# Performance work log

Hardware: AMD Instinct MI355X
Metric: run time of the kernel (lower is better)

Reference implementation:

```python
import jax, jax.numpy as jnp
import numpy as np

LAMBDA_VOLUME = 0.2
LAMBDA_WEIGHTED_ADJ = 0.15
LAMBDA_SYM = 0.05
AGE_MAX = 100.0
EPS_ROW = 1e-8
EPS_STD = 1e-6


def _smooth_l1(x):
    # F.smooth_l1_loss(x, 0) with beta=1, mean reduction
    ax = jnp.abs(x)
    return jnp.mean(jnp.where(ax < 1.0, 0.5 * x * x, ax - 0.5))


def setup_inputs() -> dict:
    key = jax.random.key(0)
    ks = jax.random.split(key, 9)
    B, C, X = 2, 32, 96
    logits = jax.random.normal(ks[0], (B, C, X, X, X), dtype=jnp.float32)
    age = jax.random.uniform(ks[1], (B, 1), dtype=jnp.float32) * AGE_MAX
    w_young = jax.random.uniform(ks[2], (C, C), dtype=jnp.float32)
    w_old = jax.random.uniform(ks[3], (C, C), dtype=jnp.float32)
    # expected per-class volumes ~ total_voxels / C in scale
    vol_means_young = jax.random.uniform(ks[4], (C,), dtype=jnp.float32) * 50000.0
    vol_means_old = jax.random.uniform(ks[5], (C,), dtype=jnp.float32) * 50000.0
    vol_stds_young = jax.random.uniform(ks[6], (C,), dtype=jnp.float32) * 5000.0 + 1000.0
    vol_stds_old = jax.random.uniform(ks[7], (C,), dtype=jnp.float32) * 5000.0 + 1000.0
    prior_adj = jax.random.uniform(ks[8], (C, C), dtype=jnp.float32)
    # left-right pair permutation: class i <-> i + C//2
    perm = jnp.concatenate([jnp.arange(C // 2, C), jnp.arange(0, C // 2)]).astype(jnp.int64)
    return {"logits": logits, "age": age, "w_young": w_young, "w_old": w_old,
            "vol_means_young": vol_means_young, "vol_means_old": vol_means_old,
            "vol_stds_young": vol_stds_young, "vol_stds_old": vol_stds_old,
            "prior_adj": prior_adj, "perm": perm}


def reference(logits, age, w_young, w_old, vol_means_young, vol_means_old,
              vol_stds_young, vol_stds_old, prior_adj, perm):
    B, C = logits.shape[0], logits.shape[1]
    probs = jax.nn.softmax(logits, axis=1)  # (B,C,X,Y,Z)
    alpha = jnp.clip(age / AGE_MAX, 0.0, 1.0)  # (B,1) interpolation between age anchors

    # ---- weighted adjacency loss (temperature == 1.0 -> no pow) ----
    pf = probs.reshape(B, C, -1)                     # (B,C,N)
    A = jnp.einsum('bcn,bdn->bcd', pf, pf)           # bmm(probs, probs^T)
    A = A * (1.0 - jnp.eye(C, dtype=A.dtype))        # zero diagonal
    W = (1.0 - alpha)[:, :, None] * w_young[None] + alpha[:, :, None] * w_old[None]  # (B,C,C)
    A = A * W
    Aw = A.mean(axis=0)
    Aw = Aw / jnp.clip(Aw.sum(axis=1, keepdims=True), EPS_ROW)
    prior = prior_adj * (1.0 - jnp.eye(C, dtype=prior_adj.dtype))
    prior = prior / jnp.clip(prior.sum(axis=1, keepdims=True), EPS_ROW)
    loss_adj = jnp.mean(jnp.abs(Aw - prior))

    # ---- volume consistency loss ----
    pred_vol = probs.sum(axis=(2, 3, 4))             # (B,C)
    means = (1.0 - alpha) * vol_means_young[None] + alpha * vol_means_old[None]
    stds = (1.0 - alpha) * vol_stds_young[None] + alpha * vol_stds_old[None]
    loss_vol = _smooth_l1((pred_vol - means) / (stds + EPS_STD))

    # ---- symmetry consistency loss (flip along X axis = dim 2, swap LR pairs) ----
    p_flip = jnp.flip(probs, axis=2)
    p_swap = p_flip[:, perm]                         # channel permutation = pairwise swap
    loss_sym = jnp.mean(jnp.abs(probs - p_swap))

    total = (LAMBDA_WEIGHTED_ADJ * loss_adj
             + LAMBDA_VOLUME * loss_vol
             + LAMBDA_SYM * loss_sym)
    return total
```

## Files before the change

kernel.cpp:

```cpp
#include <hip/hip_runtime.h>
#include <math.h>

#define CX 32
#define XX 9216
#define X3 884736
#define TILE_PAIRS 128
#define TILES_PER_B 3456
#define BLOCKS_PER_B 384
#define STRIDE 257


__global__ __launch_bounds__(256, 3)
void main_pass(const float* __restrict__ logits,
               float* __restrict__ A_acc,
               float* __restrict__ pvol_acc,
               float* __restrict__ sym_acc)
{
    __shared__ float lds[CX * STRIDE];
    const int tid = threadIdx.x;
    const int b   = blockIdx.x / BLOCKS_PER_B;
    const int blk = blockIdx.x % BLOCKS_PER_B;
    const float* lg = logits + (size_t)b * (size_t)(CX * X3);

    float acc[8][8];
#pragma unroll
    for (int i = 0; i < 8; ++i)
#pragma unroll
        for (int j = 0; j < 8; ++j) acc[i][j] = 0.f;
    float pvol[CX];
#pragma unroll
    for (int c = 0; c < CX; ++c) pvol[c] = 0.f;
    float sym = 0.f;

    const int g  = tid >> 4;
    const int s  = tid & 15;
    const int c0 = (s >> 2) * 8;
    const int d0 = (s & 3) * 8;
    const int half = tid & 127;
    const bool isB = tid >= 128;

    for (int tile = blk; tile < TILES_PER_B; tile += BLOCKS_PER_B) {
        int i   = tile * TILE_PAIRS + half;
        int x   = i / XX;
        int rem = i - x * XX;
        int xx  = isB ? (95 - x) : x;
        int off = xx * XX + rem;

        float p[CX];
#pragma unroll
        for (int c = 0; c < CX; ++c) p[c] = lg[off + c * X3];
        float m = p[0];
#pragma unroll
        for (int c = 1; c < CX; ++c) m = fmaxf(m, p[c]);
        float ssum = 0.f;
#pragma unroll
        for (int c = 0; c < CX; ++c) { p[c] = __expf(p[c] - m); ssum += p[c]; }
        float inv = 1.f / ssum;
#pragma unroll
        for (int c = 0; c < CX; ++c) {
            p[c] *= inv;
            pvol[c] += p[c];
            lds[c * STRIDE + tid] = p[c];
        }
        __syncthreads();

        if (!isB) {
#pragma unroll
            for (int c = 0; c < CX; ++c)
                sym += fabsf(p[c] - lds[((c + 16) & 31) * STRIDE + 128 + tid]);
        }

#pragma unroll 4
        for (int k = 0; k < 16; ++k) {
            int n = (k << 4) + g;
            float av[8], bv[8];
#pragma unroll
            for (int ii = 0; ii < 8; ++ii) av[ii] = lds[(c0 + ii) * STRIDE + n];
#pragma unroll
            for (int jj = 0; jj < 8; ++jj) bv[jj] = lds[(d0 + jj) * STRIDE + n];
#pragma unroll
            for (int ii = 0; ii < 8; ++ii)
#pragma unroll
                for (int jj = 0; jj < 8; ++jj)
                    acc[ii][jj] += av[ii] * bv[jj];
        }
        __syncthreads();
    }

    for (int w = 8; w >= 1; w >>= 1) {
        int lim = w * 16;
        if (tid >= lim && tid < 2 * lim) {
#pragma unroll
            for (int v = 0; v < 64; ++v)
                lds[(tid - lim) * 64 + v] = acc[v >> 3][v & 7];
        }
        __syncthreads();
        if (tid < lim) {
#pragma unroll
            for (int v = 0; v < 64; ++v)
                acc[v >> 3][v & 7] += lds[tid * 64 + v];
        }
        __syncthreads();
    }
    if (tid < 16) {
        float* Ab = A_acc + b * (CX * CX);
#pragma unroll
        for (int v = 0; v < 64; ++v) {
            int c = c0 + (v >> 3);
            int d = d0 + (v & 7);
            atomicAdd(&Ab[c * CX + d], acc[v >> 3][v & 7]);
        }
    }
    __syncthreads();

#pragma unroll
    for (int c = 0; c < CX; ++c) lds[c * 256 + tid] = pvol[c];
    __syncthreads();
    {
        int c = tid >> 3, j = tid & 7;
        float v = 0.f;
#pragma unroll
        for (int k = 0; k < 32; ++k) v += lds[c * 256 + j * 32 + k];
        v += __shfl_down(v, 4, 8);
        v += __shfl_down(v, 2, 8);
        v += __shfl_down(v, 1, 8);
        if (j == 0) atomicAdd(&pvol_acc[b * CX + c], v);
    }

    float sv = sym;
#pragma unroll
    for (int off = 32; off >= 1; off >>= 1) sv += __shfl_down(sv, off);
    __syncthreads();
    if ((tid & 63) == 0) lds[tid >> 6] = sv;
    __syncthreads();
    if (tid == 0) atomicAdd(sym_acc, lds[0] + lds[1] + lds[2] + lds[3]);
}

__global__ void finalize(const float* __restrict__ A_acc,
                         const float* __restrict__ pvol,
                         const float* __restrict__ sym,
                         const float* __restrict__ age,
                         const float* __restrict__ wy,  const float* __restrict__ wo,
                         const float* __restrict__ vmy, const float* __restrict__ vmo,
                         const float* __restrict__ vsy, const float* __restrict__ vso,
                         const float* __restrict__ prior,
                         float* __restrict__ out)
{
    const int t = threadIdx.x;
    float a0 = fminf(fmaxf(age[0] * 0.01f, 0.f), 1.f);
    float a1 = fminf(fmaxf(age[1] * 0.01f, 0.f), 1.f);

    float part_adj = 0.f;
    if (t < 32) {
        int c = t;
        float awrow[CX], prow[CX];
        float rs = 0.f, ps = 0.f;
#pragma unroll
        for (int d = 0; d < CX; ++d) {
            float v = 0.f, pv = 0.f;
            if (d != c) {
                float A0v = A_acc[c * CX + d];
                float A1v = A_acc[CX * CX + c * CX + d];
                float w0 = (1.f - a0) * wy[c * CX + d] + a0 * wo[c * CX + d];
                float w1 = (1.f - a1) * wy[c * CX + d] + a1 * wo[c * CX + d];
                v  = 0.5f * (A0v * w0 + A1v * w1);
                pv = prior[c * CX + d];
            }
            awrow[d] = v;  rs += v;
            prow[d]  = pv; ps += pv;
        }
        rs = fmaxf(rs, 1e-8f);
        ps = fmaxf(ps, 1e-8f);
#pragma unroll
        for (int d = 0; d < CX; ++d)
            part_adj += fabsf(awrow[d] / rs - prow[d] / ps);
    }

    float part_vol;
    {
        int bb = t >> 5, c = t & 31;
        float al = bb ? a1 : a0;
        float mean = (1.f - al) * vmy[c] + al * vmo[c];
        float sd   = (1.f - al) * vsy[c] + al * vso[c] + 1e-6f;
        float r  = (pvol[bb * CX + c] - mean) / sd;
        float ar = fabsf(r);
        part_vol = (ar < 1.f) ? 0.5f * r * r : (ar - 0.5f);
    }

#pragma unroll
    for (int off = 32; off >= 1; off >>= 1) {
        part_adj += __shfl_down(part_adj, off);
        part_vol += __shfl_down(part_vol, off);
    }
    if (t == 0) {
        float loss_adj = part_adj * (1.f / 1024.f);
        float loss_vol = part_vol * (1.f / 64.f);
        float loss_sym = sym[0] * 2.f / 56623104.f;
        out[0] = 0.15f * loss_adj + 0.2f * loss_vol + 0.05f * loss_sym;
    }
}

extern "C" void kernel_launch(void* const* d_in, const int* in_sizes, int n_in,
                              void* d_out, int out_size, void* d_ws, size_t ws_size,
                              hipStream_t stream) {
    const float* logits = (const float*)d_in[0];
    const float* age    = (const float*)d_in[1];
    const float* wy     = (const float*)d_in[2];
    const float* wo     = (const float*)d_in[3];
    const float* vmy    = (const float*)d_in[4];
    const float* vmo    = (const float*)d_in[5];
    const float* vsy    = (const float*)d_in[6];
    const float* vso    = (const float*)d_in[7];
    const float* prior  = (const float*)d_in[8];

    float* ws    = (float*)d_ws;
    float* A_acc = ws;
    float* pvol  = ws + 2048;
    float* sym   = ws + 2112;

    hipMemsetAsync(d_ws, 0, 2113 * sizeof(float), stream);
    main_pass<<<2 * BLOCKS_PER_B, 256, 0, stream>>>(logits, A_acc, pvol, sym);
    finalize<<<1, 64, 0, stream>>>(A_acc, pvol, sym, age, wy, wo,
                                   vmy, vmo, vsy, vso, prior, (float*)d_out);
}
```

Measured before the change: 446.8 us.

## Store softmax tile row-major in LDS with float2 access and fold volume into GEMM loop

Changes the shared-memory tile from channel-major (stride 257) to voxel-major rows padded to 34 floats, so writes, the symmetry read and the outer-product operand loads use float2 vector accesses. The per-thread 32-register volume accumulator becomes an 8-register one that sums the A-operand values inside the outer-product loop, followed by a reduction that divides by 4 to undo the duplicate counting across d0 groups. This cuts register pressure and LDS instruction count, but the 64-bit LDS accesses with padded rows may hit bank conflicts, and the LDS footprint rises slightly.

```diff
diff --git a/kernel.cpp b/kernel.cpp
--- a/kernel.cpp
+++ b/kernel.cpp
@@ -7,7 +7,7 @@
 #define TILE_PAIRS 128
 #define TILES_PER_B 3456
 #define BLOCKS_PER_B 384
-#define STRIDE 257
+#define RSTRIDE 34
 
 
 __global__ __launch_bounds__(256, 3)
@@ -16,7 +16,7 @@
                float* __restrict__ pvol_acc,
                float* __restrict__ sym_acc)
 {
-    __shared__ float lds[CX * STRIDE];
+    __shared__ float lds[256 * RSTRIDE];
     const int tid = threadIdx.x;
     const int b   = blockIdx.x / BLOCKS_PER_B;
     const int blk = blockIdx.x % BLOCKS_PER_B;
@@ -27,9 +27,9 @@
     for (int i = 0; i < 8; ++i)
 #pragma unroll
         for (int j = 0; j < 8; ++j) acc[i][j] = 0.f;
-    float pvol[CX];
-#pragma unroll
-    for (int c = 0; c < CX; ++c) pvol[c] = 0.f;
+    float pvol8[8];
+#pragma unroll
+    for (int i = 0; i < 8; ++i) pvol8[i] = 0.f;
     float sym = 0.f;
 
     const int g  = tid >> 4;
@@ -44,11 +44,11 @@
         int x   = i / XX;
         int rem = i - x * XX;
         int xx  = isB ? (95 - x) : x;
-        int off = xx * XX + rem;
+        size_t off = (size_t)xx * XX + (size_t)rem;
 
         float p[CX];
 #pragma unroll
-        for (int c = 0; c < CX; ++c) p[c] = lg[off + c * X3];
+        for (int c = 0; c < CX; ++c) p[c] = lg[off + (size_t)c * X3];
         float m = p[0];
 #pragma unroll
         for (int c = 1; c < CX; ++c) m = fmaxf(m, p[c]);
@@ -57,48 +57,74 @@
         for (int c = 0; c < CX; ++c) { p[c] = __expf(p[c] - m); ssum += p[c]; }
         float inv = 1.f / ssum;
 #pragma unroll
-        for (int c = 0; c < CX; ++c) {
-            p[c] *= inv;
-            pvol[c] += p[c];
-            lds[c * STRIDE + tid] = p[c];
+        for (int c = 0; c < CX; ++c) p[c] *= inv;
+
+        float2* row = (float2*)(lds + tid * RSTRIDE);
+#pragma unroll
+        for (int q = 0; q < 16; ++q) {
+            float2 t; t.x = p[2 * q]; t.y = p[2 * q + 1];
+            row[q] = t;
         }
         __syncthreads();
 
         if (!isB) {
-#pragma unroll
-            for (int c = 0; c < CX; ++c)
-                sym += fabsf(p[c] - lds[((c + 16) & 31) * STRIDE + 128 + tid]);
+            const float2* prow = (const float2*)(lds + (128 + half) * RSTRIDE);
+#pragma unroll
+            for (int j = 0; j < 16; ++j) {
+                float2 t = prow[(j + 8) & 15];
+                sym += fabsf(p[2 * j] - t.x) + fabsf(p[2 * j + 1] - t.y);
+            }
         }
 
 #pragma unroll 4
         for (int k = 0; k < 16; ++k) {
             int n = (k << 4) + g;
+            const float2* col = (const float2*)(lds + n * RSTRIDE);
             float av[8], bv[8];
 #pragma unroll
-            for (int ii = 0; ii < 8; ++ii) av[ii] = lds[(c0 + ii) * STRIDE + n];
-#pragma unroll
-            for (int jj = 0; jj < 8; ++jj) bv[jj] = lds[(d0 + jj) * STRIDE + n];
-#pragma unroll
-            for (int ii = 0; ii < 8; ++ii)
+            for (int q = 0; q < 4; ++q) {
+                float2 ta = col[(c0 >> 1) + q];
+                av[2 * q] = ta.x; av[2 * q + 1] = ta.y;
+                float2 tb = col[(d0 >> 1) + q];
+                bv[2 * q] = tb.x; bv[2 * q + 1] = tb.y;
+            }
+#pragma unroll
+            for (int ii = 0; ii < 8; ++ii) {
+                pvol8[ii] += av[ii];
 #pragma unroll
                 for (int jj = 0; jj < 8; ++jj)
-                    acc[ii][jj] += av[ii] * bv[jj];
-        }
-        __syncthreads();
-    }
+                    acc[ii][jj] = fmaf(av[ii], bv[jj], acc[ii][jj]);
+            }
+        }
+        __syncthreads();
+    }
+
+#pragma unroll
+    for (int ii = 0; ii < 8; ++ii) lds[tid * 9 + ii] = pvol8[ii];
+    __syncthreads();
+    if (tid < CX) {
+        int c = tid, cc = c & 7, b4 = (c >> 3) << 2;
+        float v = 0.f;
+        for (int u = 0; u < 16; ++u)
+#pragma unroll
+            for (int w = 0; w < 4; ++w)
+                v += lds[(u * 16 + b4 + w) * 9 + cc];
+        atomicAdd(&pvol_acc[b * CX + c], 0.25f * v);
+    }
+    __syncthreads();
 
     for (int w = 8; w >= 1; w >>= 1) {
         int lim = w * 16;
         if (tid >= lim && tid < 2 * lim) {
 #pragma unroll
             for (int v = 0; v < 64; ++v)
-                lds[(tid - lim) * 64 + v] = acc[v >> 3][v & 7];
+                lds[(tid - lim) * 65 + v] = acc[v >> 3][v & 7];
         }
         __syncthreads();
         if (tid < lim) {
 #pragma unroll
             for (int v = 0; v < 64; ++v)
-                acc[v >> 3][v & 7] += lds[tid * 64 + v];
+                acc[v >> 3][v & 7] += lds[tid * 65 + v];
         }
         __syncthreads();
     }
@@ -113,24 +139,9 @@
     }
     __syncthreads();
 
-#pragma unroll
-    for (int c = 0; c < CX; ++c) lds[c * 256 + tid] = pvol[c];
-    __syncthreads();
-    {
-        int c = tid >> 3, j = tid & 7;
-        float v = 0.f;
-#pragma unroll
-        for (int k = 0; k < 32; ++k) v += lds[c * 256 + j * 32 + k];
-        v += __shfl_down(v, 4, 8);
-        v += __shfl_down(v, 2, 8);
-        v += __shfl_down(v, 1, 8);
-        if (j == 0) atomicAdd(&pvol_acc[b * CX + c], v);
-    }
-
     float sv = sym;
 #pragma unroll
-    for (int off = 32; off >= 1; off >>= 1) sv += __shfl_down(sv, off);
-    __syncthreads();
+    for (int off2 = 32; off2 >= 1; off2 >>= 1) sv += __shfl_down(sv, off2);
     if ((tid & 63) == 0) lds[tid >> 6] = sv;
     __syncthreads();
     if (tid == 0) atomicAdd(sym_acc, lds[0] + lds[1] + lds[2] + lds[3]);
```

New measurement: 426.8 us. 1.05x faster.

## Compute Gram matrix with bf16 MFMA per wave and derive volumes from row sums

Applied to the files above, without the earlier changes.

Replaces the scalar FP32 outer-product accumulation of the 32x32 probability Gram matrix with per-wave bf16 MFMA 32x32x16 instructions. Each wave stages its 64 voxel rows as packed bf16 in a double-buffered LDS slice. Per-class volumes are no longer accumulated separately; they are taken as row sums of the full Gram matrix, which works because the probabilities sum to one. The symmetry term is now computed by both halves of the wave, and the scaling is adjusted to match. This removes FP32 FMA pressure and the pvol reduction, at the cost of bf16 rounding in the adjacency, volume and mirrored symmetry values.

```diff
diff --git a/kernel.cpp b/kernel.cpp
--- a/kernel.cpp
+++ b/kernel.cpp
@@ -4,51 +4,53 @@
 #define CX 32
 #define XX 9216
 #define X3 884736
-#define TILE_PAIRS 128
-#define TILES_PER_B 3456
-#define BLOCKS_PER_B 384
-#define STRIDE 257
-
-
-__global__ __launch_bounds__(256, 3)
+#define CHUNKS_PER_B 13824
+#define WAVES_PER_B 2048
+#define NBLOCKS 1024
+#define RSU 17
+#define RS16 34
+#define SLICE_W 1088
+
+typedef short s8v __attribute__((ext_vector_type(8)));
+typedef float f32x16 __attribute__((ext_vector_type(16)));
+
+__device__ __forceinline__ unsigned bf16rne(float f) {
+    unsigned u = __float_as_uint(f);
+    return (u + (0x7fffu + ((u >> 16) & 1u))) >> 16;
+}
+
+
+__global__ __launch_bounds__(256, 4)
 void main_pass(const float* __restrict__ logits,
                float* __restrict__ A_acc,
-               float* __restrict__ pvol_acc,
                float* __restrict__ sym_acc)
 {
-    __shared__ float lds[CX * STRIDE];
+    __shared__ __align__(16) unsigned lds_u[8704];
     const int tid = threadIdx.x;
-    const int b   = blockIdx.x / BLOCKS_PER_B;
-    const int blk = blockIdx.x % BLOCKS_PER_B;
+    const int w   = tid >> 6;
+    const int l   = tid & 63;
+    const int wid = blockIdx.x * 4 + w;
+    const int b   = wid >> 11;
+    const int wb  = wid & 2047;
+    const int lane31 = l & 31;
+    const int h = l >> 5;
+
+    unsigned* const buf0 = lds_u + w * (2 * SLICE_W);
     const float* lg = logits + (size_t)b * (size_t)(CX * X3);
 
-    float acc[8][8];
-#pragma unroll
-    for (int i = 0; i < 8; ++i)
-#pragma unroll
-        for (int j = 0; j < 8; ++j) acc[i][j] = 0.f;
-    float pvol[CX];
-#pragma unroll
-    for (int c = 0; c < CX; ++c) pvol[c] = 0.f;
+    f32x16 acc = {};
     float sym = 0.f;
 
-    const int g  = tid >> 4;
-    const int s  = tid & 15;
-    const int c0 = (s >> 2) * 8;
-    const int d0 = (s & 3) * 8;
-    const int half = tid & 127;
-    const bool isB = tid >= 128;
-
-    for (int tile = blk; tile < TILES_PER_B; tile += BLOCKS_PER_B) {
-        int i   = tile * TILE_PAIRS + half;
-        int x   = i / XX;
-        int rem = i - x * XX;
-        int xx  = isB ? (95 - x) : x;
-        int off = xx * XX + rem;
+    for (int it = 0, cg = wb; cg < CHUNKS_PER_B; ++it, cg += WAVES_PER_B) {
+        unsigned* const sb = buf0 + (it & 1) * SLICE_W;
+        int x   = cg / 288;
+        int rem = (cg - x * 288) * 32 + lane31;
+        int xx  = h ? (95 - x) : x;
+        const float* gp = lg + (size_t)xx * XX + (size_t)rem;
 
         float p[CX];
 #pragma unroll
-        for (int c = 0; c < CX; ++c) p[c] = lg[off + c * X3];
+        for (int c = 0; c < CX; ++c) p[c] = gp[(size_t)c * X3];
         float m = p[0];
 #pragma unroll
         for (int c = 1; c < CX; ++c) m = fmaxf(m, p[c]);
@@ -57,87 +59,65 @@
         for (int c = 0; c < CX; ++c) { p[c] = __expf(p[c] - m); ssum += p[c]; }
         float inv = 1.f / ssum;
 #pragma unroll
-        for (int c = 0; c < CX; ++c) {
-            p[c] *= inv;
-            pvol[c] += p[c];
-            lds[c * STRIDE + tid] = p[c];
-        }
+        for (int c = 0; c < CX; ++c) p[c] *= inv;
+
+        unsigned* myrow = sb + l * RSU;
+#pragma unroll
+        for (int c2 = 0; c2 < 16; ++c2)
+            myrow[c2] = bf16rne(p[2 * c2]) | (bf16rne(p[2 * c2 + 1]) << 16);
+
         __syncthreads();
 
-        if (!isB) {
-#pragma unroll
-            for (int c = 0; c < CX; ++c)
-                sym += fabsf(p[c] - lds[((c + 16) & 31) * STRIDE + 128 + tid]);
-        }
-
-#pragma unroll 4
-        for (int k = 0; k < 16; ++k) {
-            int n = (k << 4) + g;
-            float av[8], bv[8];
-#pragma unroll
-            for (int ii = 0; ii < 8; ++ii) av[ii] = lds[(c0 + ii) * STRIDE + n];
-#pragma unroll
-            for (int jj = 0; jj < 8; ++jj) bv[jj] = lds[(d0 + jj) * STRIDE + n];
-#pragma unroll
-            for (int ii = 0; ii < 8; ++ii)
-#pragma unroll
-                for (int jj = 0; jj < 8; ++jj)
-                    acc[ii][jj] += av[ii] * bv[jj];
-        }
-        __syncthreads();
-    }
-
-    for (int w = 8; w >= 1; w >>= 1) {
-        int lim = w * 16;
-        if (tid >= lim && tid < 2 * lim) {
-#pragma unroll
-            for (int v = 0; v < 64; ++v)
-                lds[(tid - lim) * 64 + v] = acc[v >> 3][v & 7];
-        }
-        __syncthreads();
-        if (tid < lim) {
-#pragma unroll
-            for (int v = 0; v < 64; ++v)
-                acc[v >> 3][v & 7] += lds[tid * 64 + v];
-        }
-        __syncthreads();
-    }
-    if (tid < 16) {
-        float* Ab = A_acc + b * (CX * CX);
-#pragma unroll
-        for (int v = 0; v < 64; ++v) {
-            int c = c0 + (v >> 3);
-            int d = d0 + (v & 7);
-            atomicAdd(&Ab[c * CX + d], acc[v >> 3][v & 7]);
-        }
-    }
+        const unsigned* prow = sb + (l ^ 32) * RSU;
+#pragma unroll
+        for (int j = 0; j < 16; ++j) {
+            unsigned q = prow[(j + 8) & 15];
+            sym += fabsf(p[2 * j]     - __uint_as_float(q << 16));
+            sym += fabsf(p[2 * j + 1] - __uint_as_float(q & 0xffff0000u));
+        }
+
+        const unsigned short* sb16 = (const unsigned short*)sb;
+#pragma unroll
+        for (int t = 0; t < 4; ++t) {
+            s8v af;
+#pragma unroll
+            for (int j = 0; j < 8; ++j)
+                af[j] = (short)sb16[(16 * t + 8 * h + j) * RS16 + lane31];
+            acc = __builtin_amdgcn_mfma_f32_32x32x16_bf16(af, af, acc, 0, 0, 0);
+        }
+    }
+
     __syncthreads();
-
-#pragma unroll
-    for (int c = 0; c < CX; ++c) lds[c * 256 + tid] = pvol[c];
+    float* lds_f = (float*)lds_u;
+#pragma unroll
+    for (int r = 0; r < 16; ++r) {
+        int row = (r & 3) + 8 * (r >> 2) + 4 * h;
+        lds_f[w * 1056 + row * 32 + lane31] = acc[r];
+    }
+    float sv = sym;
+#pragma unroll
+    for (int o = 32; o >= 1; o >>= 1) sv += __shfl_down(sv, o);
+    if (l == 0) lds_f[4224 + w] = sv;
     __syncthreads();
+
     {
-        int c = tid >> 3, j = tid & 7;
-        float v = 0.f;
-#pragma unroll
-        for (int k = 0; k < 32; ++k) v += lds[c * 256 + j * 32 + k];
-        v += __shfl_down(v, 4, 8);
-        v += __shfl_down(v, 2, 8);
-        v += __shfl_down(v, 1, 8);
-        if (j == 0) atomicAdd(&pvol_acc[b * CX + c], v);
-    }
-
-    float sv = sym;
-#pragma unroll
-    for (int off = 32; off >= 1; off >>= 1) sv += __shfl_down(sv, off);
-    __syncthreads();
-    if ((tid & 63) == 0) lds[tid >> 6] = sv;
-    __syncthreads();
-    if (tid == 0) atomicAdd(sym_acc, lds[0] + lds[1] + lds[2] + lds[3]);
+        float4 s = make_float4(0.f, 0.f, 0.f, 0.f);
+#pragma unroll
+        for (int ww = 0; ww < 4; ++ww) {
+            const float4 v = *((const float4*)lds_f + ww * 264 + tid);
+            s.x += v.x; s.y += v.y; s.z += v.z; s.w += v.w;
+        }
+        float* Ab = A_acc + b * (CX * CX) + tid * 4;
+        atomicAdd(&Ab[0], s.x);
+        atomicAdd(&Ab[1], s.y);
+        atomicAdd(&Ab[2], s.z);
+        atomicAdd(&Ab[3], s.w);
+    }
+    if (tid == 0)
+        atomicAdd(sym_acc, lds_f[4224] + lds_f[4225] + lds_f[4226] + lds_f[4227]);
 }
 
 __global__ void finalize(const float* __restrict__ A_acc,
-                         const float* __restrict__ pvol,
                          const float* __restrict__ sym,
                          const float* __restrict__ age,
                          const float* __restrict__ wy,  const float* __restrict__ wo,
@@ -150,9 +130,23 @@
     float a0 = fminf(fmaxf(age[0] * 0.01f, 0.f), 1.f);
     float a1 = fminf(fmaxf(age[1] * 0.01f, 0.f), 1.f);
 
+    const int bb = t >> 5, c = t & 31;
+    float full = 0.f;
+#pragma unroll
+    for (int d = 0; d < CX; ++d) full += A_acc[bb * 1024 + c * CX + d];
+
+    float part_vol;
+    {
+        float al = bb ? a1 : a0;
+        float mean = (1.f - al) * vmy[c] + al * vmo[c];
+        float sd   = (1.f - al) * vsy[c] + al * vso[c] + 1e-6f;
+        float r  = (full - mean) / sd;
+        float ar = fabsf(r);
+        part_vol = (ar < 1.f) ? 0.5f * r * r : (ar - 0.5f);
+    }
+
     float part_adj = 0.f;
     if (t < 32) {
-        int c = t;
         float awrow[CX], prow[CX];
         float rs = 0.f, ps = 0.f;
 #pragma unroll
@@ -160,7 +154,7 @@
             float v = 0.f, pv = 0.f;
             if (d != c) {
                 float A0v = A_acc[c * CX + d];
-                float A1v = A_acc[CX * CX + c * CX + d];
+                float A1v = A_acc[1024 + c * CX + d];
                 float w0 = (1.f - a0) * wy[c * CX + d] + a0 * wo[c * CX + d];
                 float w1 = (1.f - a1) * wy[c * CX + d] + a1 * wo[c * CX + d];
                 v  = 0.5f * (A0v * w0 + A1v * w1);
@@ -176,17 +170,6 @@
             part_adj += fabsf(awrow[d] / rs - prow[d] / ps);
     }
 
-    float part_vol;
-    {
-        int bb = t >> 5, c = t & 31;
-        float al = bb ? a1 : a0;
-        float mean = (1.f - al) * vmy[c] + al * vmo[c];
-        float sd   = (1.f - al) * vsy[c] + al * vso[c] + 1e-6f;
-        float r  = (pvol[bb * CX + c] - mean) / sd;
-        float ar = fabsf(r);
-        part_vol = (ar < 1.f) ? 0.5f * r * r : (ar - 0.5f);
-    }
-
 #pragma unroll
     for (int off = 32; off >= 1; off >>= 1) {
         part_adj += __shfl_down(part_adj, off);
@@ -195,7 +178,7 @@
     if (t == 0) {
         float loss_adj = part_adj * (1.f / 1024.f);
         float loss_vol = part_vol * (1.f / 64.f);
-        float loss_sym = sym[0] * 2.f / 56623104.f;
+        float loss_sym = sym[0] / 56623104.f;
         out[0] = 0.15f * loss_adj + 0.2f * loss_vol + 0.05f * loss_sym;
     }
 }
@@ -215,11 +198,10 @@
 
     float* ws    = (float*)d_ws;
     float* A_acc = ws;
-    float* pvol  = ws + 2048;
-    float* sym   = ws + 2112;
-
-    hipMemsetAsync(d_ws, 0, 2113 * sizeof(float), stream);
-    main_pass<<<2 * BLOCKS_PER_B, 256, 0, stream>>>(logits, A_acc, pvol, sym);
-    finalize<<<1, 64, 0, stream>>>(A_acc, pvol, sym, age, wy, wo,
+    float* sym   = ws + 2048;
+
+    hipMemsetAsync(d_ws, 0, 2049 * sizeof(float), stream);
+    main_pass<<<NBLOCKS, 256, 0, stream>>>(logits, A_acc, sym);
+    finalize<<<1, 64, 0, stream>>>(A_acc, sym, age, wy, wo,
                                    vmy, vmo, vsy, vso, prior, (float*)d_out);
 }
```

Result: faster. 392.0 us (-12.3%).
